# Kernel optimization log

Measured on AMD Instinct MI355X. Metric: run time of the kernel, lower is better.

The kernel has to match this reference:

```python
import jax, jax.numpy as jnp
import numpy as np

_SHAPE = (4, 2, 8, 256, 513)  # N, 2(real/imag), C, T, F


def setup_inputs() -> dict:
    key = jax.random.key(0)
    k1, k2, k3 = jax.random.split(key, 3)
    return {
        "mixture": jax.random.normal(k1, _SHAPE, dtype=jnp.float32),
        "target": jax.random.normal(k2, _SHAPE, dtype=jnp.float32),
        "noise": jax.random.normal(k3, _SHAPE, dtype=jnp.float32),
        "ref_mic_idx": 0,
    }


def _to_complex(x):
    # (N, 2, C, T, F) real-imag stacked -> complex (N, C, T, F)
    return jax.lax.complex(x[:, 0], x[:, 1])


def _mean_spatial_cov(s):
    # s: complex (N, C, T, F) -> time-averaged covariance (N, F, C, C)
    N, C, T, F = s.shape
    sc = jnp.transpose(s, (0, 3, 2, 1))  # (N, F, T, C)
    # outer product V V^H summed over T, fused into one batched GEMM
    return jnp.einsum("nftc,nftd->nfcd", sc, jnp.conj(sc)) / T


def reference(mixture, target, noise, ref_mic_idx):
    y = _to_complex(mixture)  # (N, C, T, F)
    x = _to_complex(target)
    v = _to_complex(noise)
    N, C, T, F = y.shape

    phi_target = _mean_spatial_cov(x)  # (N, F, C, C)
    # diagonal loading: torch adds load to BOTH real and imag parts (RI dim broadcast)
    load = (0.001 / np.sqrt(2)) * (1.0 + 1.0j)
    phi_noise = _mean_spatial_cov(v) + jnp.asarray(load, dtype=y.dtype) * jnp.eye(C, dtype=y.dtype)

    G = jnp.linalg.inv(phi_noise) @ phi_target  # (N, F, C, C)
    l = jnp.trace(G, axis1=-2, axis2=-1)  # (N, F)
    # W = (1/l) * G @ e_ref  -> select column ref_mic_idx
    W = G[..., ref_mic_idx] / l[..., None]  # (N, F, C)

    # X_bf(n,t,f) = W^H y = sum_c conj(W)_{nfc} y_{nctf}
    X_bf = jnp.einsum("nfc,nctf->ntf", jnp.conj(W), y)  # (N, T, F)
    # restack real/imag and add singleton channel dim -> (N, 2, 1, T, F)
    out = jnp.stack([X_bf.real, X_bf.imag], axis=1)[:, :, None]
    return out
```

## Files before the change

kernel.cpp:

```cpp
#include <hip/hip_runtime.h>

#define Nn 4
#define Cc 8
#define Tt 256
#define Ff 513
#define TFs (Tt * Ff)
#define NCHUNK 16
#define TCHUNK (Tt / NCHUNK)
#define SLAB ((size_t)Ff * 72)

__global__ __launch_bounds__(256) void cov_partial(
    const float* __restrict__ target, const float* __restrict__ noise,
    float* __restrict__ partial)
{
    int tid = threadIdx.x;
    int lane = tid & 63, wave = tid >> 6;
    int f0 = blockIdx.x * 64;
    int f = f0 + lane;
    int fc = f < Ff ? f : (Ff - 1);
    int n = blockIdx.y;
    int z = blockIdx.z;
    int inp = z & 1;
    int chunk = z >> 1;

    const float* src = inp ? noise : target;
    const float* bt = src + (size_t)n * 2 * Cc * TFs
                      + (size_t)(chunk * TCHUNK + wave * 4) * Ff + fc;

    float ar[36], ai[36];
#pragma unroll
    for (int p = 0; p < 36; ++p) { ar[p] = 0.f; ai[p] = 0.f; }

#pragma unroll 2
    for (int tt = 0; tt < 4; ++tt) {
        float re[8], im[8];
#pragma unroll
        for (int c = 0; c < 8; ++c) {
            re[c] = bt[(size_t)c * TFs];
            im[c] = bt[(size_t)(Cc + c) * TFs];
        }
        int p = 0;
#pragma unroll
        for (int a = 0; a < 8; ++a) {
#pragma unroll
            for (int b = a; b < 8; ++b, ++p) {
                ar[p] += re[a] * re[b] + im[a] * im[b];
                if (a != b)
                    ai[p] += im[a] * re[b] - re[a] * im[b];
            }
        }
        bt += Ff;
    }

    __shared__ float red[2][64][73];
    int reg = wave & 1;
    if (wave < 2) {
        int p = 0;
#pragma unroll
        for (int a = 0; a < 8; ++a)
#pragma unroll
            for (int b = a; b < 8; ++b, ++p) {
                red[reg][lane][2 * p]     = ar[p];
                red[reg][lane][2 * p + 1] = (a == b) ? 0.f : ai[p];
            }
    }
    __syncthreads();
    if (wave >= 2) {
        int p = 0;
#pragma unroll
        for (int a = 0; a < 8; ++a)
#pragma unroll
            for (int b = a; b < 8; ++b, ++p) {
                red[reg][lane][2 * p] += ar[p];
                if (a != b) red[reg][lane][2 * p + 1] += ai[p];
            }
    }
    __syncthreads();

    int nf = Ff - f0; if (nf > 64) nf = 64;
    float* dst = partial + (((size_t)inp * Nn + n) * NCHUNK + chunk) * SLAB
                 + (size_t)f0 * 72;
    for (int i = tid; i < nf * 72; i += 256) {
        int fl = i / 72, j = i - fl * 72;
        dst[i] = red[0][fl][j] + red[1][fl][j];
    }
}

__global__ __launch_bounds__(64) void mvdr_weights(
    const float* __restrict__ partial, const int* __restrict__ ref_ptr,
    float2* __restrict__ wconj)
{
    int f = blockIdx.x;
    int n = blockIdx.y;
    int lane = threadIdx.x;

    int r = lane >> 3, c = lane & 7;
    int lo = r < c ? r : c, hi = r < c ? c : r;
    int p = lo * 8 - lo * (lo - 1) / 2 + (hi - lo);

    const float* pT = partial + ((size_t)(0 * Nn + n) * NCHUNK) * SLAB
                      + (size_t)f * 72 + 2 * p;
    const float* pN = partial + ((size_t)(1 * Nn + n) * NCHUNK) * SLAB
                      + (size_t)f * 72 + 2 * p;
    float2 sT = make_float2(0.f, 0.f), sN = make_float2(0.f, 0.f);
#pragma unroll
    for (int ch = 0; ch < NCHUNK; ++ch) {
        float2 vT = *(const float2*)(pT + ch * SLAB);
        float2 vN = *(const float2*)(pN + ch * SLAB);
        sT.x += vT.x; sT.y += vT.y;
        sN.x += vN.x; sN.y += vN.y;
    }

    const float invT = 1.0f / (float)Tt;
    const float dl = 0.001f / 1.41421356237309515f;
    float sgn = (r > c) ? -1.f : 1.f;

    float2 a = make_float2(sN.x * invT, sgn * sN.y * invT);
    float2 b = make_float2(sT.x * invT, sgn * sT.y * invT);
    if (r == c) { a.x += dl; a.y += dl; }

    for (int k = 0; k < 8; ++k) {
        float mag = (c == k && r >= k) ? (a.x * a.x + a.y * a.y) : -1.f;
        int midx = r;
#pragma unroll
        for (int st = 8; st < 64; st <<= 1) {
            float om = __shfl_xor(mag, st, 64);
            int   oi = __shfl_xor(midx, st, 64);
            if (om > mag) { mag = om; midx = oi; }
        }
        int piv = __shfl(midx, k, 64);

        int srcr = (r == k) ? piv : ((r == piv) ? k : r);
        int src = srcr * 8 + c;
        a.x = __shfl(a.x, src, 64); a.y = __shfl(a.y, src, 64);
        b.x = __shfl(b.x, src, 64); b.y = __shfl(b.y, src, 64);

        float pvx = __shfl(a.x, k * 8 + k, 64), pvy = __shfl(a.y, k * 8 + k, 64);
        float d = pvx * pvx + pvy * pvy;
        float ipx = pvx / d, ipy = -pvy / d;
        if (r == k) {
            float2 t = a;
            a = make_float2(t.x * ipx - t.y * ipy, t.x * ipy + t.y * ipx);
            t = b;
            b = make_float2(t.x * ipx - t.y * ipy, t.x * ipy + t.y * ipx);
        }

        float rax = __shfl(a.x, k * 8 + c, 64), ray = __shfl(a.y, k * 8 + c, 64);
        float rbx = __shfl(b.x, k * 8 + c, 64), rby = __shfl(b.y, k * 8 + c, 64);
        float fx  = __shfl(a.x, r * 8 + k, 64), fy  = __shfl(a.y, r * 8 + k, 64);
        if (r != k) {
            a.x -= fx * rax - fy * ray;  a.y -= fx * ray + fy * rax;
            b.x -= fx * rbx - fy * rby;  b.y -= fx * rby + fy * rbx;
        }
    }

    float tx = (r == c) ? b.x : 0.f, ty = (r == c) ? b.y : 0.f;
#pragma unroll
    for (int st = 1; st < 64; st <<= 1) {
        tx += __shfl_xor(tx, st, 64);
        ty += __shfl_xor(ty, st, 64);
    }

    int ref = *ref_ptr;
    if (c == ref) {
        float den = tx * tx + ty * ty;
        float wx = (b.x * tx + b.y * ty) / den;
        float wy = (b.y * tx - b.x * ty) / den;
        wconj[((size_t)n * Ff + f) * 8 + r] = make_float2(wx, -wy);
    }
}

__global__ __launch_bounds__(256) void beamform(
    const float* __restrict__ y, const float2* __restrict__ wconj,
    float* __restrict__ out)
{
    int idx = blockIdx.x * 256 + threadIdx.x;
    int n = idx / TFs;
    int rem = idx - n * TFs;
    int t = rem / Ff;
    int f = rem - t * Ff;

    size_t base_re = (size_t)n * 2 * Cc * TFs + (size_t)t * Ff + f;
    size_t base_im = base_re + (size_t)Cc * TFs;
    const float2* w = wconj + ((size_t)n * Ff + f) * 8;

    float xr = 0.f, xi = 0.f;
#pragma unroll
    for (int c = 0; c < Cc; ++c) {
        float yre = y[base_re + (size_t)c * TFs];
        float yim = y[base_im + (size_t)c * TFs];
        float2 wc = w[c];
        xr += wc.x * yre - wc.y * yim;
        xi += wc.x * yim + wc.y * yre;
    }
    size_t ob = (size_t)n * 2 * TFs + (size_t)t * Ff + f;
    out[ob] = xr;
    out[ob + TFs] = xi;
}

extern "C" void kernel_launch(void* const* d_in, const int* in_sizes, int n_in,
                              void* d_out, int out_size, void* d_ws, size_t ws_size,
                              hipStream_t stream) {
    const float* mixture = (const float*)d_in[0];
    const float* target  = (const float*)d_in[1];
    const float* noise   = (const float*)d_in[2];
    const int*   refp    = (const int*)d_in[3];
    float* out = (float*)d_out;

    float*  partial = (float*)d_ws;
    float2* wconj = (float2*)((char*)d_ws +
                              (size_t)2 * Nn * NCHUNK * SLAB * sizeof(float));

    cov_partial<<<dim3(9, Nn, NCHUNK * 2), 256, 0, stream>>>(target, noise, partial);
    mvdr_weights<<<dim3(Ff, Nn), 64, 0, stream>>>(partial, refp, wconj);
    beamform<<<dim3((Nn * TFs) / 256), 256, 0, stream>>>(mixture, wconj, out);
}
```

Measured before the change: 143.9 us.

## Split covariance work across waves by matrix row pairs instead of time

Each of the four waves now handles all 16 time steps of the chunk but only two rows of the upper-triangular 8x8 covariance (rows G and 7-G, 9 entries), rather than every entry for 4 time steps. This cuts accumulator registers from 72 to 18 per thread and removes the cross-wave shared-memory reduction and one barrier. In exchange each wave reloads the channel data it needs, so global and cache load traffic rises roughly fourfold per block, and the template dispatch branches on wave index.

```diff
diff --git a/kernel.cpp b/kernel.cpp
--- a/kernel.cpp
+++ b/kernel.cpp
@@ -8,6 +8,52 @@
 #define NCHUNK 16
 #define TCHUNK (Tt / NCHUNK)
 #define SLAB ((size_t)Ff * 72)
+
+template <int G>
+__device__ __forceinline__ void cov_group(const float* __restrict__ bt,
+                                          float (*red)[73], int lane)
+{
+    constexpr int R2 = 7 - G;
+    float ar[9], ai[9];
+#pragma unroll
+    for (int s = 0; s < 9; ++s) { ar[s] = 0.f; ai[s] = 0.f; }
+
+#pragma unroll 2
+    for (int tt = 0; tt < TCHUNK; ++tt) {
+        float re[8], im[8];
+#pragma unroll
+        for (int c = G; c < 8; ++c) {
+            re[c] = bt[(size_t)c * TFs];
+            im[c] = bt[(size_t)(Cc + c) * TFs];
+        }
+        int s = 0;
+#pragma unroll
+        for (int d = G; d < 8; ++d, ++s) {
+            ar[s] += re[G] * re[d] + im[G] * im[d];
+            if (d != G) ai[s] += im[G] * re[d] - re[G] * im[d];
+        }
+#pragma unroll
+        for (int d = R2; d < 8; ++d, ++s) {
+            ar[s] += re[R2] * re[d] + im[R2] * im[d];
+            if (d != R2) ai[s] += im[R2] * re[d] - re[R2] * im[d];
+        }
+        bt += Ff;
+    }
+
+    int s = 0;
+#pragma unroll
+    for (int d = G; d < 8; ++d, ++s) {
+        const int p = G * 8 - G * (G - 1) / 2 + (d - G);
+        red[lane][2 * p]     = ar[s];
+        red[lane][2 * p + 1] = (d == G) ? 0.f : ai[s];
+    }
+#pragma unroll
+    for (int d = R2; d < 8; ++d, ++s) {
+        const int p = R2 * 8 - R2 * (R2 - 1) / 2 + (d - R2);
+        red[lane][2 * p]     = ar[s];
+        red[lane][2 * p + 1] = (d == R2) ? 0.f : ai[s];
+    }
+}
 
 __global__ __launch_bounds__(256) void cov_partial(
     const float* __restrict__ target, const float* __restrict__ noise,
@@ -25,55 +71,14 @@
 
     const float* src = inp ? noise : target;
     const float* bt = src + (size_t)n * 2 * Cc * TFs
-                      + (size_t)(chunk * TCHUNK + wave * 4) * Ff + fc;
-
-    float ar[36], ai[36];
-#pragma unroll
-    for (int p = 0; p < 36; ++p) { ar[p] = 0.f; ai[p] = 0.f; }
-
-#pragma unroll 2
-    for (int tt = 0; tt < 4; ++tt) {
-        float re[8], im[8];
-#pragma unroll
-        for (int c = 0; c < 8; ++c) {
-            re[c] = bt[(size_t)c * TFs];
-            im[c] = bt[(size_t)(Cc + c) * TFs];
-        }
-        int p = 0;
-#pragma unroll
-        for (int a = 0; a < 8; ++a) {
-#pragma unroll
-            for (int b = a; b < 8; ++b, ++p) {
-                ar[p] += re[a] * re[b] + im[a] * im[b];
-                if (a != b)
-                    ai[p] += im[a] * re[b] - re[a] * im[b];
-            }
-        }
-        bt += Ff;
-    }
-
-    __shared__ float red[2][64][73];
-    int reg = wave & 1;
-    if (wave < 2) {
-        int p = 0;
-#pragma unroll
-        for (int a = 0; a < 8; ++a)
-#pragma unroll
-            for (int b = a; b < 8; ++b, ++p) {
-                red[reg][lane][2 * p]     = ar[p];
-                red[reg][lane][2 * p + 1] = (a == b) ? 0.f : ai[p];
-            }
-    }
-    __syncthreads();
-    if (wave >= 2) {
-        int p = 0;
-#pragma unroll
-        for (int a = 0; a < 8; ++a)
-#pragma unroll
-            for (int b = a; b < 8; ++b, ++p) {
-                red[reg][lane][2 * p] += ar[p];
-                if (a != b) red[reg][lane][2 * p + 1] += ai[p];
-            }
+                      + (size_t)(chunk * TCHUNK) * Ff + fc;
+
+    __shared__ float red[64][73];
+    switch (wave) {
+        case 0: cov_group<0>(bt, red, lane); break;
+        case 1: cov_group<1>(bt, red, lane); break;
+        case 2: cov_group<2>(bt, red, lane); break;
+        default: cov_group<3>(bt, red, lane); break;
     }
     __syncthreads();
 
@@ -82,7 +87,7 @@
                  + (size_t)f0 * 72;
     for (int i = tid; i < nf * 72; i += 256) {
         int fl = i / 72, j = i - fl * 72;
-        dst[i] = red[0][fl][j] + red[1][fl][j];
+        dst[i] = red[fl][j];
     }
 }
 
```

Result: slower. 156.8 us (+8.9%).

## Prefetch next time step in covariance loop and make weights channel-major

Applied to the files above, without the earlier changes.

The covariance kernel now software-pipelines its loads, reading the next time step's 16 values while the outer-product accumulation runs on the current one, so load latency is hidden behind FMAs. The weight buffer moves from (n,f,c) to (n,c,f), which makes beamform's per-channel weight reads coalesced across lanes instead of strided by 8 float2. The cost is higher register pressure in cov_partial, which already holds 72 accumulators.

```diff
diff --git a/kernel.cpp b/kernel.cpp
--- a/kernel.cpp
+++ b/kernel.cpp
@@ -31,25 +31,39 @@
 #pragma unroll
     for (int p = 0; p < 36; ++p) { ar[p] = 0.f; ai[p] = 0.f; }
 
-#pragma unroll 2
+    float cre[8], cim[8];
+#pragma unroll
+    for (int c = 0; c < 8; ++c) {
+        cre[c] = bt[(size_t)c * TFs];
+        cim[c] = bt[(size_t)(Cc + c) * TFs];
+    }
+
+#pragma unroll
     for (int tt = 0; tt < 4; ++tt) {
-        float re[8], im[8];
-#pragma unroll
-        for (int c = 0; c < 8; ++c) {
-            re[c] = bt[(size_t)c * TFs];
-            im[c] = bt[(size_t)(Cc + c) * TFs];
+        const float* nx = bt + Ff;
+        float pre[8], pim[8];
+        if (tt < 3) {
+#pragma unroll
+            for (int c = 0; c < 8; ++c) {
+                pre[c] = nx[(size_t)c * TFs];
+                pim[c] = nx[(size_t)(Cc + c) * TFs];
+            }
         }
         int p = 0;
 #pragma unroll
         for (int a = 0; a < 8; ++a) {
 #pragma unroll
             for (int b = a; b < 8; ++b, ++p) {
-                ar[p] += re[a] * re[b] + im[a] * im[b];
+                ar[p] += cre[a] * cre[b] + cim[a] * cim[b];
                 if (a != b)
-                    ai[p] += im[a] * re[b] - re[a] * im[b];
-            }
-        }
-        bt += Ff;
+                    ai[p] += cim[a] * cre[b] - cre[a] * cim[b];
+            }
+        }
+        if (tt < 3) {
+#pragma unroll
+            for (int c = 0; c < 8; ++c) { cre[c] = pre[c]; cim[c] = pim[c]; }
+        }
+        bt = nx;
     }
 
     __shared__ float red[2][64][73];
@@ -166,7 +180,7 @@
         float den = tx * tx + ty * ty;
         float wx = (b.x * tx + b.y * ty) / den;
         float wy = (b.y * tx - b.x * ty) / den;
-        wconj[((size_t)n * Ff + f) * 8 + r] = make_float2(wx, -wy);
+        wconj[((size_t)n * 8 + r) * Ff + f] = make_float2(wx, -wy);
     }
 }
 
@@ -182,14 +196,14 @@
 
     size_t base_re = (size_t)n * 2 * Cc * TFs + (size_t)t * Ff + f;
     size_t base_im = base_re + (size_t)Cc * TFs;
-    const float2* w = wconj + ((size_t)n * Ff + f) * 8;
+    const float2* w = wconj + (size_t)n * 8 * Ff + f;
 
     float xr = 0.f, xi = 0.f;
 #pragma unroll
     for (int c = 0; c < Cc; ++c) {
         float yre = y[base_re + (size_t)c * TFs];
         float yim = y[base_im + (size_t)c * TFs];
-        float2 wc = w[c];
+        float2 wc = w[(size_t)c * Ff];
         xr += wc.x * yre - wc.y * yim;
         xi += wc.x * yim + wc.y * yre;
     }
```

Measured after the change: 147.0 us. 1.02x slower.
